# Kernel tuning notes

Measured on AMD Instinct MI355X. Metric: run time of the kernel, lower is better.

Reference implementation:

```python
import jax, jax.numpy as jnp
import numpy as np

N = 16384      # nodes
E = 262144     # edges
H = 512        # hidden_dim
G = 256        # graphs in batch
L = 4          # num_layers - 1 conv layers
OUT = 128      # output_dim
AF, AV = 9, 128   # atom features, atom vocab per feature
BF, BV = 3, 8     # bond features, bond vocab per feature


def setup_inputs() -> dict:
    key = jax.random.key(0)
    ks = jax.random.split(key, 10)
    h_node = jax.random.randint(ks[0], (N, AF), 0, 119, dtype=jnp.int32)
    h_edge = jax.random.randint(ks[1], (E, BF), 0, 5, dtype=jnp.int32)
    src = jax.random.randint(ks[2], (E,), 0, N, dtype=jnp.int32)
    dst = jax.random.randint(ks[3], (E,), 0, N, dtype=jnp.int32)
    gid = jnp.sort(jax.random.randint(ks[4], (N,), 0, G, dtype=jnp.int32))
    atom_emb = jax.random.normal(ks[5], (AF, AV, H), dtype=jnp.float32) * 0.02
    bond_emb = jax.random.normal(ks[6], (L, BF, BV, H), dtype=jnp.float32) * 0.02
    W = jax.random.normal(ks[7], (L, H, H), dtype=jnp.float32) / np.float32(np.sqrt(H))
    b = jnp.zeros((L, H), jnp.float32)
    gn_w = jnp.ones((L, H), jnp.float32)
    gn_b = jnp.zeros((L, H), jnp.float32)
    gn_ms = jnp.ones((L, H), jnp.float32)  # GraphNorm mean_scale (alpha)
    Wp = jax.random.normal(ks[8], (H, OUT), dtype=jnp.float32) / np.float32(np.sqrt(H))
    bp = jnp.zeros((OUT,), jnp.float32)
    return dict(h_node=h_node, h_edge=h_edge, src=src, dst=dst, gid=gid,
                atom_emb=atom_emb, bond_emb=bond_emb, W=W, b=b,
                gn_w=gn_w, gn_b=gn_b, gn_ms=gn_ms, Wp=Wp, bp=bp)


def _multi_embed_sum(tbl, idx, nfeat, vocab):
    # tbl: [nfeat, vocab, H], idx: [M, nfeat] -> sum of per-feature embeddings [M, H]
    flat = tbl.reshape(nfeat * vocab, tbl.shape[-1])
    off = idx + (jnp.arange(nfeat, dtype=idx.dtype) * vocab)[None, :]
    return flat[off].sum(axis=1)


def _graph_norm(h, gid, w, bb, ms):
    # GraphNorm: weight * (h - alpha*mean_g) / std_g + bias, per graph
    cnt = jax.ops.segment_sum(jnp.ones((h.shape[0],), h.dtype), gid, num_segments=G)
    cnt = jnp.maximum(cnt, 1.0)[:, None]
    mean = jax.ops.segment_sum(h, gid, num_segments=G) / cnt
    sub = h - mean[gid] * ms
    var = jax.ops.segment_sum(sub * sub, gid, num_segments=G) / cnt
    return w * sub / jnp.sqrt(var + 1e-6)[gid] + bb


def reference(h_node, h_edge, src, dst, gid, atom_emb, bond_emb, W, b,
              gn_w, gn_b, gn_ms, Wp, bp):
    h = _multi_embed_sum(atom_emb, h_node, AF, AV)  # AtomEncoder -> [N, H]
    ones_e = jnp.ones((E,), h.dtype)
    indeg = jnp.maximum(jax.ops.segment_sum(ones_e, dst, num_segments=N), 1.0)[:, None]
    for i in range(L):
        x = h
        he = _multi_embed_sum(bond_emb[i], h_edge, BF, BV)  # BondEncoder -> [E, H]
        msg = h[src] + he                                   # u_add_e
        neigh = jax.ops.segment_sum(msg, dst, num_segments=N) / indeg  # mean reduce
        r = h + neigh                                       # (1 + eps)*x + neigh, eps=0
        r = r @ W[i] + b[i]                                 # MLP (1-layer linear)
        r = _graph_norm(r, gid, gn_w[i], gn_b[i], gn_ms[i])
        if i != L - 1:
            r = jax.nn.relu(r)
        h = r + x                                           # residual
    pooled = jax.ops.segment_sum(h, gid, num_segments=G)    # SumPooling -> [G, H]
    return pooled @ Wp + bp                                 # [G, OUT] (dropout = eval identity)
```

## Files before the change

### kernel.cpp

```cpp
#include <hip/hip_runtime.h>

#define N_NODES 16384
#define N_EDGES 262144
#define HID 512
#define NG 256
#define NL 4
#define NOUT 128

typedef __attribute__((ext_vector_type(8))) short bf16x8;
typedef __attribute__((ext_vector_type(4))) float f32x4;
typedef __attribute__((ext_vector_type(8))) unsigned short u16x8;

static __device__ __forceinline__ unsigned short f2bf(float f) {
    unsigned int u = __float_as_uint(f);
    unsigned int r = (u + 0x7fffu + ((u >> 16) & 1u)) >> 16;
    return (unsigned short)r;
}
static __device__ __forceinline__ float bf2f(unsigned short s) {
    return __uint_as_float(((unsigned int)s) << 16);
}

static __device__ __forceinline__ void gload_lds16(const unsigned short* g, unsigned short* l) {
    __builtin_amdgcn_global_load_lds(
        (const __attribute__((address_space(1))) unsigned int*)(g),
        (__attribute__((address_space(3))) unsigned int*)(l), 16, 0, 0);
}

__global__ __launch_bounds__(256) void k_prep(const int* __restrict__ hn, const float* __restrict__ aemb,
                                              unsigned short* __restrict__ h_bf,
                                              const int* __restrict__ dst, int* __restrict__ cnt,
                                              const float* __restrict__ W, unsigned short* __restrict__ Wt,
                                              const float* __restrict__ bemb, unsigned short* __restrict__ ctab,
                                              const int* __restrict__ gid, int* __restrict__ gs,
                                              float* __restrict__ rcnt) {
    const int bid = blockIdx.x;
    const int tid = threadIdx.x;
    if (bid < 8192) {
        int n = bid * 2 + (tid >> 7);
        int c = (tid & 127) * 4;
        float4 acc = make_float4(0.f, 0.f, 0.f, 0.f);
        for (int f = 0; f < 9; ++f) {
            int v = hn[n * 9 + f];
            const float4 ev = *(const float4*)(aemb + (size_t)(f * 128 + v) * HID + c);
            acc.x += ev.x; acc.y += ev.y; acc.z += ev.z; acc.w += ev.w;
        }
        ushort4 pk;
        pk.x = f2bf(acc.x); pk.y = f2bf(acc.y); pk.z = f2bf(acc.z); pk.w = f2bf(acc.w);
        *(ushort4*)(h_bf + (size_t)n * HID + c) = pk;
    } else if (bid < 9216) {
        int e = (bid - 8192) * 256 + tid;
        atomicAdd(&cnt[dst[e]], 1);
    } else if (bid < 13312) {
        int id = (bid - 9216) * 256 + tid;
        int l = id >> 18;
        int n = (id >> 9) & 511;
        int k = id & 511;
        Wt[id] = f2bf(W[((size_t)l << 18) + ((size_t)k << 9) + n]);
    } else if (bid < 17408) {
        int id = (bid - 13312) * 256 + tid;
        int c = id & 511;
        int combo = (id >> 9) & 511;
        int l = id >> 18;
        int i0 = combo >> 6, i1 = (combo >> 3) & 7, i2 = combo & 7;
        const float* bl = bemb + (size_t)l * 3 * 8 * HID;
        float v = bl[(size_t)i0 * HID + c] + bl[(size_t)(8 + i1) * HID + c] + bl[(size_t)(16 + i2) * HID + c];
        ctab[id] = f2bf(v);
    } else {
        int g = tid;
        int lo = 0, hi = N_NODES;
        while (lo < hi) { int mid = (lo + hi) >> 1; if (gid[mid] < g) lo = mid + 1; else hi = mid; }
        gs[g] = lo;
        if (g == 0) gs[NG] = N_NODES;
        __syncthreads();
        int e = (g == NG - 1) ? N_NODES : gs[g + 1];
        rcnt[g] = 1.0f / fmaxf((float)(e - lo), 1.0f);
    }
}

__global__ void k_scan(const int* __restrict__ cnt, int* __restrict__ rs) {
    __shared__ int spre[256];
    int t = threadIdx.x;
    int base = t * 64;
    int s = 0;
    for (int i = 0; i < 64; ++i) s += cnt[base + i];
    spre[t] = s;
    __syncthreads();
    if (t == 0) {
        int run = 0;
        for (int i = 0; i < 256; ++i) { int v = spre[i]; spre[i] = run; run += v; }
        rs[N_NODES] = run;
    }
    __syncthreads();
    int run = spre[t];
    for (int i = 0; i < 64; ++i) { rs[base + i] = run; run += cnt[base + i]; }
}

__global__ void k_fillep(const int* __restrict__ dst, const int* __restrict__ rs,
                         int* __restrict__ fc, const int* __restrict__ src,
                         const int* __restrict__ hedge, int2* __restrict__ ep) {
    int e = blockIdx.x * 256 + threadIdx.x;
    int d = dst[e];
    int pos = atomicAdd(&fc[d], 1);
    int s = src[e];
    int c = hedge[e * 3 + 0] * 64 + hedge[e * 3 + 1] * 8 + hedge[e * 3 + 2];
    ep[rs[d] + pos] = make_int2(s << 10, c << 10);
}

__global__ __launch_bounds__(256) void k_neigh(const unsigned short* __restrict__ h_bf,
                                               const int2* __restrict__ ep,
                                               const int* __restrict__ rs,
                                               const unsigned short* __restrict__ ctab,
                                               unsigned short* __restrict__ t) {
    int bid = blockIdx.x;
    int slice = (bid >> 1) & 3;
    int ng = (bid >> 3) * 2 + (bid & 1);
    int wave = threadIdx.x >> 6;
    int lane = threadIdx.x & 63;
    int eo = lane >> 4;
    int cl = lane & 15;
    int n = ng * 4 + wave;
    int cb = slice * 256 + cl * 16;
    const char* hb = (const char*)h_bf;
    const char* cbt = (const char*)ctab;
    int s = rs[n], e = rs[n + 1];
    float acc[8] = {0.f, 0.f, 0.f, 0.f, 0.f, 0.f, 0.f, 0.f};
    int j = s + eo;
    for (; j + 4 < e; j += 8) {
        int2 p0 = ep[j];
        int2 p1 = ep[j + 4];
        u16x8 a0 = *(const u16x8*)(hb + (unsigned)(p0.x + cb));
        u16x8 b0 = *(const u16x8*)(cbt + (unsigned)(p0.y + cb));
        u16x8 a1 = *(const u16x8*)(hb + (unsigned)(p1.x + cb));
        u16x8 b1 = *(const u16x8*)(cbt + (unsigned)(p1.y + cb));
        #pragma unroll
        for (int q = 0; q < 8; ++q)
            acc[q] += (bf2f(a0[q]) + bf2f(b0[q])) + (bf2f(a1[q]) + bf2f(b1[q]));
    }
    if (j < e) {
        int2 p0 = ep[j];
        u16x8 a0 = *(const u16x8*)(hb + (unsigned)(p0.x + cb));
        u16x8 b0 = *(const u16x8*)(cbt + (unsigned)(p0.y + cb));
        #pragma unroll
        for (int q = 0; q < 8; ++q)
            acc[q] += bf2f(a0[q]) + bf2f(b0[q]);
    }
    #pragma unroll
    for (int q = 0; q < 8; ++q) {
        acc[q] += __shfl_xor(acc[q], 16, 64);
        acc[q] += __shfl_xor(acc[q], 32, 64);
    }
    if (eo == 0) {
        u16x8 hself = *(const u16x8*)(hb + (size_t)n * 1024 + cb);
        float inv = 1.0f / fmaxf((float)(e - s), 1.0f);
        u16x8 pk;
        #pragma unroll
        for (int q = 0; q < 8; ++q)
            pk[q] = f2bf(bf2f(hself[q]) + acc[q] * inv);
        *(u16x8*)((char*)t + (size_t)n * 1024 + cb) = pk;
    }
}

#define BM 128
#define BN 128
#define BK 64

__global__ __launch_bounds__(256) void k_gemm(const unsigned short* __restrict__ A,
                                              const unsigned short* __restrict__ Bt,
                                              const float* __restrict__ bias,
                                              unsigned short* __restrict__ C) {
    __shared__ unsigned short As[BM * BK];
    __shared__ unsigned short Bs[BN * BK];
    const int tid = threadIdx.x;
    const int m0 = blockIdx.x * BM;
    const int n0 = blockIdx.y * BN;
    const int w = tid >> 6, lane = tid & 63;
    const int wm = (w >> 1) * 64, wn = (w & 1) * 64;
    const int lr = lane & 15, lg = lane >> 4;

    const int srow = tid >> 3;
    const int scol = ((tid & 7) ^ (srow & 7)) * 8;

    f32x4 acc[4][4] = {};

    for (int k0 = 0; k0 < HID; k0 += BK) {
        __syncthreads();
        #pragma unroll
        for (int r = 0; r < 4; ++r)
            gload_lds16(A + (size_t)(m0 + r * 32 + srow) * HID + k0 + scol,
                        As + r * 2048 + w * 512);
        #pragma unroll
        for (int r = 0; r < 4; ++r)
            gload_lds16(Bt + (size_t)(n0 + r * 32 + srow) * HID + k0 + scol,
                        Bs + r * 2048 + w * 512);
        __syncthreads();

        #pragma unroll
        for (int kk = 0; kk < 2; ++kk) {
            bf16x8 af[4], bfr[4];
            #pragma unroll
            for (int i = 0; i < 4; ++i) {
                int row = wm + i * 16 + lr;
                af[i] = *(const bf16x8*)(As + row * BK + (((kk * 4 + lg) ^ (row & 7)) * 8));
            }
            #pragma unroll
            for (int j = 0; j < 4; ++j) {
                int row = wn + j * 16 + lr;
                bfr[j] = *(const bf16x8*)(Bs + row * BK + (((kk * 4 + lg) ^ (row & 7)) * 8));
            }
            #pragma unroll
            for (int i = 0; i < 4; ++i)
                #pragma unroll
                for (int j = 0; j < 4; ++j)
                    acc[i][j] = __builtin_amdgcn_mfma_f32_16x16x32_bf16(af[i], bfr[j], acc[i][j], 0, 0, 0);
        }
    }

    #pragma unroll
    for (int i = 0; i < 4; ++i) {
        const int grow = m0 + wm + i * 16 + lg * 4;
        #pragma unroll
        for (int j = 0; j < 4; ++j) {
            const int gcol = n0 + wn + j * 16 + lr;
            const float bv = bias[gcol];
            #pragma unroll
            for (int rr = 0; rr < 4; ++rr)
                C[(size_t)(grow + rr) * HID + gcol] = f2bf(acc[i][j][rr] + bv);
        }
    }
}

__global__ __launch_bounds__(256) void k_gstats(const unsigned short* __restrict__ r,
                                                const int* __restrict__ gs,
                                                float* __restrict__ psum, float* __restrict__ psq) {
    int g = blockIdx.x;
    int seg = blockIdx.y;
    int s = gs[g], e = gs[g + 1];
    int c = threadIdx.x * 2;
    float s0 = 0.f, s1 = 0.f, q0 = 0.f, q1 = 0.f;
    for (int n = s + seg; n < e; n += 8) {
        ushort2 v = *(const ushort2*)(r + (size_t)n * HID + c);
        float v0 = bf2f(v.x), v1 = bf2f(v.y);
        s0 += v0; s1 += v1; q0 += v0 * v0; q1 += v1 * v1;
    }
    size_t o = ((size_t)seg * NG + g) * HID + c;
    *(float2*)(psum + o) = make_float2(s0, s1);
    *(float2*)(psq + o) = make_float2(q0, q1);
}

__global__ __launch_bounds__(256) void k_gred(const float* __restrict__ psum, const float* __restrict__ psq,
                                              float* __restrict__ gsum, float* __restrict__ gsq) {
    int idx = blockIdx.x * 256 + threadIdx.x;
    float s = 0.f, q = 0.f;
    #pragma unroll
    for (int seg = 0; seg < 8; ++seg) {
        s += psum[(size_t)seg * NG * HID + idx];
        q += psq[(size_t)seg * NG * HID + idx];
    }
    gsum[idx] = s;
    gsq[idx] = q;
}

__global__ __launch_bounds__(256) void k_gapply(const unsigned short* __restrict__ r,
                                                unsigned short* __restrict__ h_bf,
                                                const int* __restrict__ gid,
                                                const float* __restrict__ rcnt,
                                                const float* __restrict__ gsum, const float* __restrict__ gsq,
                                                const float* __restrict__ gw, const float* __restrict__ gb,
                                                const float* __restrict__ gms) {
    int n = blockIdx.x * 2 + (threadIdx.x >> 7);
    int c = (threadIdx.x & 127) * 4;
    int g = gid[n];
    float rc = rcnt[g];
    const float4 sm = *(const float4*)(gsum + (size_t)g * HID + c);
    const float4 sq = *(const float4*)(gsq + (size_t)g * HID + c);
    const float4 ms = *(const float4*)(gms + c);
    const float4 gwv = *(const float4*)(gw + c);
    const float4 gbv = *(const float4*)(gb + c);
    const ushort4 rv4 = *(const ushort4*)(r + (size_t)n * HID + c);
    const ushort4 hv4 = *(const ushort4*)(h_bf + (size_t)n * HID + c);
    float rv[4] = {bf2f(rv4.x), bf2f(rv4.y), bf2f(rv4.z), bf2f(rv4.w)};
    float hv[4] = {bf2f(hv4.x), bf2f(hv4.y), bf2f(hv4.z), bf2f(hv4.w)};
    float outv[4];
    float mean, am, var, wgt, v;
    #define CH(X, K)                                                \
        mean = sm.X * rc; am = ms.X * mean;                         \
        var = sq.X * rc - 2.f * am * mean + am * am;                \
        wgt = gwv.X * rsqrtf(var + 1e-6f);                          \
        v = (rv[K] - am) * wgt + gbv.X;                             \
        v = fmaxf(v, 0.f);                                          \
        outv[K] = v + hv[K];
    CH(x, 0)
    CH(y, 1)
    CH(z, 2)
    CH(w, 3)
    #undef CH
    ushort4 pk;
    pk.x = f2bf(outv[0]); pk.y = f2bf(outv[1]); pk.z = f2bf(outv[2]); pk.w = f2bf(outv[3]);
    *(ushort4*)(h_bf + (size_t)n * HID + c) = pk;
}

__global__ __launch_bounds__(256) void k_gpool(const unsigned short* __restrict__ r,
                                               const unsigned short* __restrict__ h_bf,
                                               const int* __restrict__ gs,
                                               const float* __restrict__ rcnt,
                                               const float* __restrict__ gsum, const float* __restrict__ gsq,
                                               const float* __restrict__ gw, const float* __restrict__ gb,
                                               const float* __restrict__ gms,
                                               float* __restrict__ ppool) {
    int g = blockIdx.x;
    int seg = blockIdx.y;
    int s = gs[g], e = gs[g + 1];
    int c = threadIdx.x * 2;
    float rc = rcnt[g];
    float2 sm = *(const float2*)(gsum + (size_t)g * HID + c);
    float2 sq = *(const float2*)(gsq + (size_t)g * HID + c);
    float2 ms = *(const float2*)(gms + c);
    float2 gwv = *(const float2*)(gw + c);
    float2 gbv = *(const float2*)(gb + c);
    float mean0 = sm.x * rc, am0 = ms.x * mean0;
    float var0 = sq.x * rc - 2.f * am0 * mean0 + am0 * am0;
    float wgt0 = gwv.x * rsqrtf(var0 + 1e-6f);
    float mean1 = sm.y * rc, am1 = ms.y * mean1;
    float var1 = sq.y * rc - 2.f * am1 * mean1 + am1 * am1;
    float wgt1 = gwv.y * rsqrtf(var1 + 1e-6f);
    float p0 = 0.f, p1 = 0.f;
    for (int n = s + seg; n < e; n += 8) {
        ushort2 rv = *(const ushort2*)(r + (size_t)n * HID + c);
        ushort2 hv = *(const ushort2*)(h_bf + (size_t)n * HID + c);
        p0 += (bf2f(rv.x) - am0) * wgt0 + gbv.x + bf2f(hv.x);
        p1 += (bf2f(rv.y) - am1) * wgt1 + gbv.y + bf2f(hv.y);
    }
    size_t o = ((size_t)seg * NG + g) * HID + c;
    *(float2*)(ppool + o) = make_float2(p0, p1);
}

__global__ __launch_bounds__(128) void k_proj(const float* __restrict__ ppool,
                                              const float* __restrict__ Wp,
                                              const float* __restrict__ bp, float* __restrict__ out) {
    int g = blockIdx.x;
    int tid = threadIdx.x;
    __shared__ float pr[HID];
    {
        int c = tid * 4;
        float4 sv = make_float4(0.f, 0.f, 0.f, 0.f);
        #pragma unroll
        for (int seg = 0; seg < 8; ++seg) {
            const float4 v = *(const float4*)(ppool + ((size_t)seg * NG + g) * HID + c);
            sv.x += v.x; sv.y += v.y; sv.z += v.z; sv.w += v.w;
        }
        *(float4*)(pr + c) = sv;
    }
    __syncthreads();
    int o = tid;
    float acc = bp[o];
    #pragma unroll 8
    for (int k = 0; k < HID; ++k) acc += pr[k] * Wp[k * NOUT + o];
    out[g * NOUT + o] = acc;
}

extern "C" void kernel_launch(void* const* d_in, const int* in_sizes, int n_in,
                              void* d_out, int out_size, void* d_ws, size_t ws_size,
                              hipStream_t stream) {
    const int*   h_node = (const int*)d_in[0];
    const int*   h_edge = (const int*)d_in[1];
    const int*   src    = (const int*)d_in[2];
    const int*   dst    = (const int*)d_in[3];
    const int*   gid    = (const int*)d_in[4];
    const float* aemb   = (const float*)d_in[5];
    const float* bemb   = (const float*)d_in[6];
    const float* W      = (const float*)d_in[7];
    const float* bias   = (const float*)d_in[8];
    const float* gnw    = (const float*)d_in[9];
    const float* gnb    = (const float*)d_in[10];
    const float* gnms   = (const float*)d_in[11];
    const float* Wp     = (const float*)d_in[12];
    const float* bp     = (const float*)d_in[13];
    float* out = (float*)d_out;

    char* ws = (char*)d_ws;
    size_t off = 0;
    auto alloc = [&](size_t bytes) -> char* {
        char* p = ws + off;
        off += (bytes + 255) & ~(size_t)255;
        return p;
    };
    int* cnt            = (int*)alloc((size_t)N_NODES * 4);
    int* fc             = (int*)alloc((size_t)N_NODES * 4);
    size_t zbytes = off;

    unsigned short* h_bf= (unsigned short*)alloc((size_t)N_NODES * HID * 2);
    unsigned short* rbf = (unsigned short*)alloc((size_t)N_NODES * HID * 2);
    unsigned short* t   = (unsigned short*)alloc((size_t)N_NODES * HID * 2);
    unsigned short* Wt  = (unsigned short*)alloc((size_t)NL * HID * HID * 2);
    unsigned short* ctab= (unsigned short*)alloc((size_t)NL * 512 * HID * 2);
    int2* ep            = (int2*)alloc((size_t)N_EDGES * 8);
    int* rs             = (int*)alloc((size_t)(N_NODES + 1) * 4);
    int* gs             = (int*)alloc((size_t)(NG + 1) * 4);
    float* rcnt         = (float*)alloc((size_t)NG * 4);
    float* pstat        = (float*)alloc((size_t)2 * 8 * NG * HID * 4);
    float* gstat        = (float*)alloc((size_t)2 * NG * HID * 4);
    float* ppool        = (float*)alloc((size_t)8 * NG * HID * 4);
    float* psum = pstat;
    float* psq  = pstat + (size_t)8 * NG * HID;
    float* gsum = gstat;
    float* gsq  = gstat + (size_t)NG * HID;

    hipMemsetAsync(cnt, 0, zbytes, stream);
    k_prep<<<17409, 256, 0, stream>>>(h_node, aemb, h_bf, dst, cnt, W, Wt, bemb, ctab,
                                      gid, gs, rcnt);
    k_scan<<<1, 256, 0, stream>>>(cnt, rs);
    k_fillep<<<N_EDGES / 256, 256, 0, stream>>>(dst, rs, fc, src, h_edge, ep);

    for (int i = 0; i < NL; ++i) {
        k_neigh<<<16384, 256, 0, stream>>>(h_bf, ep, rs,
                                           ctab + (size_t)i * 512 * HID, t);
        dim3 gg(N_NODES / BM, HID / BN);
        k_gemm<<<gg, 256, 0, stream>>>(t, Wt + (size_t)i * HID * HID, bias + i * HID, rbf);
        k_gstats<<<dim3(NG, 8), 256, 0, stream>>>(rbf, gs, psum, psq);
        k_gred<<<NG * HID / 256, 256, 0, stream>>>(psum, psq, gsum, gsq);
        if (i < NL - 1) {
            k_gapply<<<N_NODES / 2, 256, 0, stream>>>(rbf, h_bf, gid, rcnt, gsum, gsq,
                                                      gnw + i * HID, gnb + i * HID, gnms + i * HID);
        } else {
            k_gpool<<<dim3(NG, 8), 256, 0, stream>>>(rbf, h_bf, gs, rcnt, gsum, gsq,
                                                     gnw + i * HID, gnb + i * HID, gnms + i * HID,
                                                     ppool);
        }
    }
    k_proj<<<NG, NOUT, 0, stream>>>(ppool, Wp, bp, out);
}
```

Baseline: 380.3 us.

## Gather neighbor features and bond table in FP8 for message aggregation

Result: faster. 362.9 us (-4.6%).

```diff
diff --git a/kernel.cpp b/kernel.cpp
--- a/kernel.cpp
+++ b/kernel.cpp
@@ -19,6 +19,17 @@
 static __device__ __forceinline__ float bf2f(unsigned short s) {
     return __uint_as_float(((unsigned int)s) << 16);
 }
+static __device__ __forceinline__ unsigned int f8pk4(float a, float b, float c, float d) {
+    int r = __builtin_amdgcn_cvt_pk_fp8_f32(a, b, 0, false);
+    r = __builtin_amdgcn_cvt_pk_fp8_f32(c, d, r, true);
+    return (unsigned int)r;
+}
+static __device__ __forceinline__ void dec8(unsigned int wa, unsigned int wb, float* a) {
+    a[0] += __builtin_amdgcn_cvt_f32_fp8(wa, 0) + __builtin_amdgcn_cvt_f32_fp8(wb, 0);
+    a[1] += __builtin_amdgcn_cvt_f32_fp8(wa, 1) + __builtin_amdgcn_cvt_f32_fp8(wb, 1);
+    a[2] += __builtin_amdgcn_cvt_f32_fp8(wa, 2) + __builtin_amdgcn_cvt_f32_fp8(wb, 2);
+    a[3] += __builtin_amdgcn_cvt_f32_fp8(wa, 3) + __builtin_amdgcn_cvt_f32_fp8(wb, 3);
+}
 
 static __device__ __forceinline__ void gload_lds16(const unsigned short* g, unsigned short* l) {
     __builtin_amdgcn_global_load_lds(
@@ -28,9 +39,10 @@
 
 __global__ __launch_bounds__(256) void k_prep(const int* __restrict__ hn, const float* __restrict__ aemb,
                                               unsigned short* __restrict__ h_bf,
+                                              unsigned char* __restrict__ h_f8,
                                               const int* __restrict__ dst, int* __restrict__ cnt,
                                               const float* __restrict__ W, unsigned short* __restrict__ Wt,
-                                              const float* __restrict__ bemb, unsigned short* __restrict__ ctab,
+                                              const float* __restrict__ bemb, unsigned char* __restrict__ ctab8,
                                               const int* __restrict__ gid, int* __restrict__ gs,
                                               float* __restrict__ rcnt) {
     const int bid = blockIdx.x;
@@ -47,6 +59,7 @@
         ushort4 pk;
         pk.x = f2bf(acc.x); pk.y = f2bf(acc.y); pk.z = f2bf(acc.z); pk.w = f2bf(acc.w);
         *(ushort4*)(h_bf + (size_t)n * HID + c) = pk;
+        *(unsigned int*)(h_f8 + (size_t)n * HID + c) = f8pk4(acc.x, acc.y, acc.z, acc.w);
     } else if (bid < 9216) {
         int e = (bid - 8192) * 256 + tid;
         atomicAdd(&cnt[dst[e]], 1);
@@ -64,7 +77,8 @@
         int i0 = combo >> 6, i1 = (combo >> 3) & 7, i2 = combo & 7;
         const float* bl = bemb + (size_t)l * 3 * 8 * HID;
         float v = bl[(size_t)i0 * HID + c] + bl[(size_t)(8 + i1) * HID + c] + bl[(size_t)(16 + i2) * HID + c];
-        ctab[id] = f2bf(v);
+        int w = __builtin_amdgcn_cvt_pk_fp8_f32(v, 0.f, 0, false);
+        ctab8[id] = (unsigned char)(w & 0xff);
     } else {
         int g = tid;
         int lo = 0, hi = N_NODES;
@@ -103,60 +117,72 @@
     int pos = atomicAdd(&fc[d], 1);
     int s = src[e];
     int c = hedge[e * 3 + 0] * 64 + hedge[e * 3 + 1] * 8 + hedge[e * 3 + 2];
-    ep[rs[d] + pos] = make_int2(s << 10, c << 10);
-}
-
-__global__ __launch_bounds__(256) void k_neigh(const unsigned short* __restrict__ h_bf,
+    ep[rs[d] + pos] = make_int2(s << 9, c << 9);
+}
+
+__global__ __launch_bounds__(256) void k_neigh(const unsigned char* __restrict__ h_f8,
+                                               const unsigned short* __restrict__ h_bf,
                                                const int2* __restrict__ ep,
                                                const int* __restrict__ rs,
-                                               const unsigned short* __restrict__ ctab,
+                                               const unsigned char* __restrict__ ctab8,
                                                unsigned short* __restrict__ t) {
     int bid = blockIdx.x;
-    int slice = (bid >> 1) & 3;
-    int ng = (bid >> 3) * 2 + (bid & 1);
+    int slice = (bid >> 2) & 1;
+    int ng = (bid >> 3) * 4 + (bid & 3);
     int wave = threadIdx.x >> 6;
     int lane = threadIdx.x & 63;
     int eo = lane >> 4;
     int cl = lane & 15;
     int n = ng * 4 + wave;
     int cb = slice * 256 + cl * 16;
-    const char* hb = (const char*)h_bf;
-    const char* cbt = (const char*)ctab;
+    const unsigned char* h8 = h_f8;
+    const unsigned char* c8 = ctab8;
     int s = rs[n], e = rs[n + 1];
-    float acc[8] = {0.f, 0.f, 0.f, 0.f, 0.f, 0.f, 0.f, 0.f};
+    float acc[16] = {};
     int j = s + eo;
     for (; j + 4 < e; j += 8) {
         int2 p0 = ep[j];
         int2 p1 = ep[j + 4];
-        u16x8 a0 = *(const u16x8*)(hb + (unsigned)(p0.x + cb));
-        u16x8 b0 = *(const u16x8*)(cbt + (unsigned)(p0.y + cb));
-        u16x8 a1 = *(const u16x8*)(hb + (unsigned)(p1.x + cb));
-        u16x8 b1 = *(const u16x8*)(cbt + (unsigned)(p1.y + cb));
-        #pragma unroll
-        for (int q = 0; q < 8; ++q)
-            acc[q] += (bf2f(a0[q]) + bf2f(b0[q])) + (bf2f(a1[q]) + bf2f(b1[q]));
+        uint4 wa0 = *(const uint4*)(h8 + (unsigned)(p0.x + cb));
+        uint4 wb0 = *(const uint4*)(c8 + (unsigned)(p0.y + cb));
+        uint4 wa1 = *(const uint4*)(h8 + (unsigned)(p1.x + cb));
+        uint4 wb1 = *(const uint4*)(c8 + (unsigned)(p1.y + cb));
+        dec8(wa0.x, wb0.x, acc);
+        dec8(wa0.y, wb0.y, acc + 4);
+        dec8(wa0.z, wb0.z, acc + 8);
+        dec8(wa0.w, wb0.w, acc + 12);
+        dec8(wa1.x, wb1.x, acc);
+        dec8(wa1.y, wb1.y, acc + 4);
+        dec8(wa1.z, wb1.z, acc + 8);
+        dec8(wa1.w, wb1.w, acc + 12);
     }
     if (j < e) {
-        int2 p0 = ep[j];
-        u16x8 a0 = *(const u16x8*)(hb + (unsigned)(p0.x + cb));
-        u16x8 b0 = *(const u16x8*)(cbt + (unsigned)(p0.y + cb));
-        #pragma unroll
-        for (int q = 0; q < 8; ++q)
-            acc[q] += bf2f(a0[q]) + bf2f(b0[q]);
+        int2 p = ep[j];
+        uint4 wa = *(const uint4*)(h8 + (unsigned)(p.x + cb));
+        uint4 wb = *(const uint4*)(c8 + (unsigned)(p.y + cb));
+        dec8(wa.x, wb.x, acc);
+        dec8(wa.y, wb.y, acc + 4);
+        dec8(wa.z, wb.z, acc + 8);
+        dec8(wa.w, wb.w, acc + 12);
     }
     #pragma unroll
-    for (int q = 0; q < 8; ++q) {
+    for (int q = 0; q < 16; ++q) {
         acc[q] += __shfl_xor(acc[q], 16, 64);
         acc[q] += __shfl_xor(acc[q], 32, 64);
     }
     if (eo == 0) {
-        u16x8 hself = *(const u16x8*)(hb + (size_t)n * 1024 + cb);
+        size_t ob = (size_t)n * 1024 + slice * 512 + cl * 32;
+        u16x8 hs0 = *(const u16x8*)((const char*)h_bf + ob);
+        u16x8 hs1 = *(const u16x8*)((const char*)h_bf + ob + 16);
         float inv = 1.0f / fmaxf((float)(e - s), 1.0f);
-        u16x8 pk;
-        #pragma unroll
-        for (int q = 0; q < 8; ++q)
-            pk[q] = f2bf(bf2f(hself[q]) + acc[q] * inv);
-        *(u16x8*)((char*)t + (size_t)n * 1024 + cb) = pk;
+        u16x8 pk0, pk1;
+        #pragma unroll
+        for (int q = 0; q < 8; ++q) {
+            pk0[q] = f2bf(bf2f(hs0[q]) + acc[q] * inv);
+            pk1[q] = f2bf(bf2f(hs1[q]) + acc[8 + q] * inv);
+        }
+        *(u16x8*)((char*)t + ob) = pk0;
+        *(u16x8*)((char*)t + ob + 16) = pk1;
     }
 }
 
@@ -262,6 +288,7 @@
 
 __global__ __launch_bounds__(256) void k_gapply(const unsigned short* __restrict__ r,
                                                 unsigned short* __restrict__ h_bf,
+                                                unsigned char* __restrict__ h_f8,
                                                 const int* __restrict__ gid,
                                                 const float* __restrict__ rcnt,
                                                 const float* __restrict__ gsum, const float* __restrict__ gsq,
@@ -297,6 +324,7 @@
     ushort4 pk;
     pk.x = f2bf(outv[0]); pk.y = f2bf(outv[1]); pk.z = f2bf(outv[2]); pk.w = f2bf(outv[3]);
     *(ushort4*)(h_bf + (size_t)n * HID + c) = pk;
+    *(unsigned int*)(h_f8 + (size_t)n * HID + c) = f8pk4(outv[0], outv[1], outv[2], outv[3]);
 }
 
 __global__ __launch_bounds__(256) void k_gpool(const unsigned short* __restrict__ r,
@@ -389,10 +417,11 @@
     size_t zbytes = off;
 
     unsigned short* h_bf= (unsigned short*)alloc((size_t)N_NODES * HID * 2);
+    unsigned char* h_f8 = (unsigned char*)alloc((size_t)N_NODES * HID);
     unsigned short* rbf = (unsigned short*)alloc((size_t)N_NODES * HID * 2);
     unsigned short* t   = (unsigned short*)alloc((size_t)N_NODES * HID * 2);
     unsigned short* Wt  = (unsigned short*)alloc((size_t)NL * HID * HID * 2);
-    unsigned short* ctab= (unsigned short*)alloc((size_t)NL * 512 * HID * 2);
+    unsigned char* ctab8= (unsigned char*)alloc((size_t)NL * 512 * HID);
     int2* ep            = (int2*)alloc((size_t)N_EDGES * 8);
     int* rs             = (int*)alloc((size_t)(N_NODES + 1) * 4);
     int* gs             = (int*)alloc((size_t)(NG + 1) * 4);
@@ -406,20 +435,20 @@
     float* gsq  = gstat + (size_t)NG * HID;
 
     hipMemsetAsync(cnt, 0, zbytes, stream);
-    k_prep<<<17409, 256, 0, stream>>>(h_node, aemb, h_bf, dst, cnt, W, Wt, bemb, ctab,
+    k_prep<<<17409, 256, 0, stream>>>(h_node, aemb, h_bf, h_f8, dst, cnt, W, Wt, bemb, ctab8,
                                       gid, gs, rcnt);
     k_scan<<<1, 256, 0, stream>>>(cnt, rs);
     k_fillep<<<N_EDGES / 256, 256, 0, stream>>>(dst, rs, fc, src, h_edge, ep);
 
     for (int i = 0; i < NL; ++i) {
-        k_neigh<<<16384, 256, 0, stream>>>(h_bf, ep, rs,
-                                           ctab + (size_t)i * 512 * HID, t);
+        k_neigh<<<8192, 256, 0, stream>>>(h_f8, h_bf, ep, rs,
+                                          ctab8 + (size_t)i * 512 * HID, t);
         dim3 gg(N_NODES / BM, HID / BN);
         k_gemm<<<gg, 256, 0, stream>>>(t, Wt + (size_t)i * HID * HID, bias + i * HID, rbf);
         k_gstats<<<dim3(NG, 8), 256, 0, stream>>>(rbf, gs, psum, psq);
         k_gred<<<NG * HID / 256, 256, 0, stream>>>(psum, psq, gsum, gsq);
         if (i < NL - 1) {
-            k_gapply<<<N_NODES / 2, 256, 0, stream>>>(rbf, h_bf, gid, rcnt, gsum, gsq,
+            k_gapply<<<N_NODES / 2, 256, 0, stream>>>(rbf, h_bf, h_f8, gid, rcnt, gsum, gsq,
                                                       gnw + i * HID, gnb + i * HID, gnms + i * HID);
         } else {
             k_gpool<<<dim3(NG, 8), 256, 0, stream>>>(rbf, h_bf, gs, rcnt, gsum, gsq,
```
